# Kernel tuning notes

Hardware: AMD Instinct MI355X
Metric: run time of the kernel (lower is better)

## Reference

```python
import jax, jax.numpy as jnp
import numpy as np

B, C, F = 16384, 1000, 256
ALPHA = 10


def setup_inputs() -> dict:
    key = jax.random.key(0)
    k1, k2, k3, k4, k5 = jax.random.split(key, 5)
    logits = jax.random.normal(k1, (B, C), dtype=jnp.float32)
    features = jax.random.normal(k2, (B, F), dtype=jnp.float32)
    mean_vecs = jax.random.normal(k3, (C, F), dtype=jnp.float32)
    # Per-class Weibull (shape, loc, scale) as fit by scipy.weibull_min.fit.
    wb_shape = jax.random.uniform(k4, (C,), dtype=jnp.float32, minval=1.0, maxval=4.0)
    wb_loc = jnp.zeros((C,), dtype=jnp.float32)
    # typical tail distance for randn features/means is ~sqrt(2F) ~ 22.6
    wb_scale = jax.random.uniform(k5, (C,), dtype=jnp.float32, minval=10.0, maxval=25.0)
    return {"logits": logits, "features": features, "mean_vecs": mean_vecs,
            "wb_shape": wb_shape, "wb_loc": wb_loc, "wb_scale": wb_scale}


def reference(logits, features, mean_vecs, wb_shape, wb_loc, wb_scale):
    # Batched per-class Euclidean distances via the GEMM identity
    # ||f - m||^2 = ||f||^2 + ||m||^2 - 2 f.m  (avoids [B,C,F] intermediate).
    f2 = jnp.sum(features * features, axis=1, keepdims=True)        # [B,1]
    m2 = jnp.sum(mean_vecs * mean_vecs, axis=1)                     # [C]
    d2 = f2 + m2[None, :] - 2.0 * (features @ mean_vecs.T)          # [B,C]
    dist = jnp.sqrt(jnp.maximum(d2, 1e-12))                         # [B,C]
    # Analytic weibull_min CDF: 1 - exp(-((x - loc)/scale)^c), 0 for x <= loc.
    xp = (dist - wb_loc[None, :]) / wb_scale[None, :]
    pos = xp > 0
    xp_safe = jnp.where(pos, xp, 1.0)
    w = jnp.where(pos, 1.0 - jnp.exp(-(xp_safe ** wb_shape[None, :])), 0.0)
    # OpenMax reweighting + softmax (exp/sum-normalize as in the original).
    scores = logits * (1.0 - w ** ALPHA)                            # [B,C]
    return jax.nn.softmax(scores, axis=-1)
```

## Files before the change

kernel.cpp:

```cpp
#include <hip/hip_runtime.h>

#define NB 16384
#define NC 1000
#define NF 256

typedef _Float16 half8 __attribute__((ext_vector_type(8)));
typedef float f32x4 __attribute__((ext_vector_type(4)));

__global__ __launch_bounds__(256) void prep_kernel(
    const float* __restrict__ mean_vecs,
    const float* __restrict__ wb_shape,
    const float* __restrict__ wb_loc,
    const float* __restrict__ wb_scale,
    _Float16* __restrict__ m16f,
    float* __restrict__ pm2,
    float* __restrict__ psh,
    float* __restrict__ pli,
    float* __restrict__ pis)
{
    const int lane = threadIdx.x & 63;
    const int W = blockIdx.x * 4 + (threadIdx.x >> 6);

    if (W < 512) {
        const int gt = W >> 3, kk = W & 7;
        int cls = gt * 16 + (lane & 15);
        if (cls > NC - 1) cls = NC - 1;
        const float* src = mean_vecs + (size_t)cls * NF + kk * 32 + (lane >> 4) * 8;
        const float4 lo = *(const float4*)src;
        const float4 hi = *(const float4*)(src + 4);
        half8 h;
        h[0]=(_Float16)lo.x; h[1]=(_Float16)lo.y; h[2]=(_Float16)lo.z; h[3]=(_Float16)lo.w;
        h[4]=(_Float16)hi.x; h[5]=(_Float16)hi.y; h[6]=(_Float16)hi.z; h[7]=(_Float16)hi.w;
        *((half8*)m16f + (size_t)W * 64 + lane) = h;
    }
    if (W < NC) {
        const float4 v = *((const float4*)(mean_vecs + (size_t)W * NF) + lane);
        float s = v.x*v.x + v.y*v.y + v.z*v.z + v.w*v.w;
        #pragma unroll
        for (int off = 1; off < 64; off <<= 1) s += __shfl_xor(s, off, 64);
        if (lane == 0) {
            const float isc = 1.0f / wb_scale[W];
            pm2[W] = s;
            psh[W] = wb_shape[W];
            pli[W] = wb_loc[W] * isc;
            pis[W] = isc;
        }
    }
}

__global__ __launch_bounds__(512, 4) void score_kernel(
    const float* __restrict__ logits,
    const float* __restrict__ features,
    const _Float16* __restrict__ m16f,
    const float* __restrict__ pm2,
    const float* __restrict__ psh,
    const float* __restrict__ pli,
    const float* __restrict__ pis,
    float* __restrict__ out)
{
    __shared__ float ssum[8][16];

    const int lane = threadIdx.x & 63;
    const int wave = threadIdx.x >> 6;
    const int q    = lane >> 4;
    const int mr   = lane & 15;
    const int row  = blockIdx.x * 16 + mr;

    half8 bfrag[8];
    float f2 = 0.f;
    const float* fb = features + (size_t)row * NF;
    #pragma unroll
    for (int kk = 0; kk < 8; ++kk) {
        const float4* p = (const float4*)(fb + kk * 32 + q * 8);
        const float4 lo = p[0], hi = p[1];
        f2 += lo.x*lo.x + lo.y*lo.y + lo.z*lo.z + lo.w*lo.w
            + hi.x*hi.x + hi.y*hi.y + hi.z*hi.z + hi.w*hi.w;
        half8 b;
        b[0]=(_Float16)lo.x; b[1]=(_Float16)lo.y; b[2]=(_Float16)lo.z; b[3]=(_Float16)lo.w;
        b[4]=(_Float16)hi.x; b[5]=(_Float16)hi.y; b[6]=(_Float16)hi.z; b[7]=(_Float16)hi.w;
        bfrag[kk] = b;
    }
    f2 += __shfl_xor(f2, 16, 64);
    f2 += __shfl_xor(f2, 32, 64);

    const float LOG2E = 1.44269504088896340736f;
    float rsum = 0.f;
    f32x4 ev[8];

    const half8* mbase = (const half8*)m16f + (size_t)(wave * 8) * 8 * 64 + lane;

    #pragma unroll
    for (int t = 0; t < 8; ++t) {
        const int gt  = wave * 8 + t;
        const int cb  = gt * 16 + q * 4;
        const bool cvg = (cb <= NC - 4);
        const int cbc = cvg ? cb : (NC - 4);

        half8 a[8];
        #pragma unroll
        for (int kk = 0; kk < 8; ++kk)
            a[kk] = mbase[(size_t)(t * 8 + kk) * 64];

        f32x4 acc = {0.f, 0.f, 0.f, 0.f};
        #pragma unroll
        for (int kk = 0; kk < 8; ++kk)
            acc = __builtin_amdgcn_mfma_f32_16x16x32_f16(a[kk], bfrag[kk], acc, 0, 0, 0);

        const float4 lg  = *(const float4*)(logits + (size_t)row * NC + cbc);
        const float4 m2v = *(const float4*)(pm2 + cbc);
        const float4 shv = *(const float4*)(psh + cbc);
        const float4 liv = *(const float4*)(pli + cbc);
        const float4 iv  = *(const float4*)(pis + cbc);

        const float* m2a = (const float*)&m2v;
        const float* sha = (const float*)&shv;
        const float* lia = (const float*)&liv;
        const float* iva = (const float*)&iv;
        const float* lga = (const float*)&lg;

        #pragma unroll
        for (int j = 0; j < 4; ++j) {
            float d2   = fmaxf(f2 + m2a[j] - 2.0f * acc[j], 1e-12f);
            float dist = sqrtf(d2);
            float xp   = dist * iva[j] - lia[j];
            float xs   = fmaxf(xp, 1e-30f);
            float tt   = exp2f(sha[j] * log2f(xs));
            float w    = 1.0f - exp2f(-LOG2E * tt);
            w = (xp > 0.f) ? w : 0.f;
            float w2 = w * w, w4 = w2 * w2, w8 = w4 * w4;
            float s  = lga[j] * (1.0f - w8 * w2);
            float e  = exp2f(LOG2E * s);
            e = cvg ? e : 0.f;
            rsum += e;
            ev[t][j] = e;
        }
    }

    rsum += __shfl_xor(rsum, 16, 64);
    rsum += __shfl_xor(rsum, 32, 64);
    if (lane < 16) ssum[wave][lane] = rsum;
    __syncthreads();
    float tot = 0.f;
    #pragma unroll
    for (int w = 0; w < 8; ++w) tot += ssum[w][mr];
    const float inv = 1.0f / tot;

    #pragma unroll
    for (int t = 0; t < 8; ++t) {
        const int gt = wave * 8 + t;
        const int cb = gt * 16 + q * 4;
        if (cb <= NC - 4) {
            float4 o;
            o.x = ev[t][0] * inv; o.y = ev[t][1] * inv;
            o.z = ev[t][2] * inv; o.w = ev[t][3] * inv;
            *(float4*)(out + (size_t)row * NC + cb) = o;
        }
    }
}

extern "C" void kernel_launch(void* const* d_in, const int* in_sizes, int n_in,
                              void* d_out, int out_size, void* d_ws, size_t ws_size,
                              hipStream_t stream) {
    const float* logits    = (const float*)d_in[0];
    const float* features  = (const float*)d_in[1];
    const float* mean_vecs = (const float*)d_in[2];
    const float* wb_shape  = (const float*)d_in[3];
    const float* wb_loc    = (const float*)d_in[4];
    const float* wb_scale  = (const float*)d_in[5];
    float* out = (float*)d_out;

    _Float16* m16f = (_Float16*)d_ws;
    float* pm2 = (float*)((char*)d_ws + 524288);
    float* psh = (float*)((char*)d_ws + 524288 + 4096);
    float* pli = (float*)((char*)d_ws + 524288 + 8192);
    float* pis = (float*)((char*)d_ws + 524288 + 12288);

    prep_kernel<<<252, 256, 0, stream>>>(mean_vecs, wb_shape, wb_loc, wb_scale,
                                         m16f, pm2, psh, pli, pis);
    score_kernel<<<NB / 16, 512, 0, stream>>>(logits, features, m16f,
                                              pm2, psh, pli, pis, out);
}
```

Measured before the change: 185.5 us.

## Stage softmax numerators in LDS for coalesced row stores; prefetch next tile

The unnormalized exponentials now go into a 16x1004 shared-memory tile instead of registers. After the row sums are reduced, each wave writes two full output rows with contiguous float4 stores, replacing the scattered 16-byte-per-lane pattern. The loop also software-prefetches the next tile's mean-vector fragments and logits while the current MFMA and epilogue run. In exchange it uses about 64KB of LDS per block, which may lower occupancy below the launch bound of 4 blocks, and adds a second barrier.

```diff
diff --git a/kernel.cpp b/kernel.cpp
--- a/kernel.cpp
+++ b/kernel.cpp
@@ -3,6 +3,7 @@
 #define NB 16384
 #define NC 1000
 #define NF 256
+#define SE_STRIDE 1004
 
 typedef _Float16 half8 __attribute__((ext_vector_type(8)));
 typedef float f32x4 __attribute__((ext_vector_type(4)));
@@ -58,7 +59,9 @@
     const float* __restrict__ pis,
     float* __restrict__ out)
 {
+    __shared__ float se[16][SE_STRIDE];
     __shared__ float ssum[8][16];
+    __shared__ float sinv[16];
 
     const int lane = threadIdx.x & 63;
     const int wave = threadIdx.x >> 6;
@@ -85,28 +88,38 @@
 
     const float LOG2E = 1.44269504088896340736f;
     float rsum = 0.f;
-    f32x4 ev[8];
 
     const half8* mbase = (const half8*)m16f + (size_t)(wave * 8) * 8 * 64 + lane;
+    const float* lrow  = logits + (size_t)row * NC;
+
+    half8 a[8];
+    #pragma unroll
+    for (int kk = 0; kk < 8; ++kk)
+        a[kk] = mbase[kk * 64];
+    float4 lg = *(const float4*)(lrow + (wave * 128 + q * 4));
 
     #pragma unroll
     for (int t = 0; t < 8; ++t) {
-        const int gt  = wave * 8 + t;
-        const int cb  = gt * 16 + q * 4;
+        const int gt   = wave * 8 + t;
+        const int cb   = gt * 16 + q * 4;
         const bool cvg = (cb <= NC - 4);
-        const int cbc = cvg ? cb : (NC - 4);
-
-        half8 a[8];
-        #pragma unroll
-        for (int kk = 0; kk < 8; ++kk)
-            a[kk] = mbase[(size_t)(t * 8 + kk) * 64];
+        const int cbc  = cvg ? cb : (NC - 4);
 
         f32x4 acc = {0.f, 0.f, 0.f, 0.f};
         #pragma unroll
         for (int kk = 0; kk < 8; ++kk)
             acc = __builtin_amdgcn_mfma_f32_16x16x32_f16(a[kk], bfrag[kk], acc, 0, 0, 0);
 
-        const float4 lg  = *(const float4*)(logits + (size_t)row * NC + cbc);
+        float4 lgn = lg;
+        if (t < 7) {
+            #pragma unroll
+            for (int kk = 0; kk < 8; ++kk)
+                a[kk] = mbase[(size_t)((t + 1) * 8 + kk) * 64];
+            const int cbn  = cb + 16;
+            const int cbnc = (cbn <= NC - 4) ? cbn : (NC - 4);
+            lgn = *(const float4*)(lrow + cbnc);
+        }
+
         const float4 m2v = *(const float4*)(pm2 + cbc);
         const float4 shv = *(const float4*)(psh + cbc);
         const float4 liv = *(const float4*)(pli + cbc);
@@ -118,6 +131,7 @@
         const float* iva = (const float*)&iv;
         const float* lga = (const float*)&lg;
 
+        f32x4 o;
         #pragma unroll
         for (int j = 0; j < 4; ++j) {
             float d2   = fmaxf(f2 + m2a[j] - 2.0f * acc[j], 1e-12f);
@@ -132,28 +146,40 @@
             float e  = exp2f(LOG2E * s);
             e = cvg ? e : 0.f;
             rsum += e;
-            ev[t][j] = e;
-        }
+            o[j] = e;
+        }
+
+        if (cvg)
+            *(f32x4*)&se[mr][cb] = o;
+
+        lg = lgn;
     }
 
     rsum += __shfl_xor(rsum, 16, 64);
     rsum += __shfl_xor(rsum, 32, 64);
     if (lane < 16) ssum[wave][lane] = rsum;
     __syncthreads();
-    float tot = 0.f;
-    #pragma unroll
-    for (int w = 0; w < 8; ++w) tot += ssum[w][mr];
-    const float inv = 1.0f / tot;
-
-    #pragma unroll
-    for (int t = 0; t < 8; ++t) {
-        const int gt = wave * 8 + t;
-        const int cb = gt * 16 + q * 4;
-        if (cb <= NC - 4) {
-            float4 o;
-            o.x = ev[t][0] * inv; o.y = ev[t][1] * inv;
-            o.z = ev[t][2] * inv; o.w = ev[t][3] * inv;
-            *(float4*)(out + (size_t)row * NC + cb) = o;
+    if (wave == 0 && lane < 16) {
+        float tot = 0.f;
+        #pragma unroll
+        for (int w = 0; w < 8; ++w) tot += ssum[w][lane];
+        sinv[lane] = 1.0f / tot;
+    }
+    __syncthreads();
+
+    #pragma unroll
+    for (int rr = 0; rr < 2; ++rr) {
+        const int r = wave * 2 + rr;
+        const float inv = sinv[r];
+        float* orow = out + (size_t)(blockIdx.x * 16 + r) * NC;
+        #pragma unroll
+        for (int i = 0; i < 4; ++i) {
+            const int idx = i * 64 + lane;
+            if (idx < 250) {
+                float4 v = *(const float4*)&se[r][idx * 4];
+                v.x *= inv; v.y *= inv; v.z *= inv; v.w *= inv;
+                *(float4*)(orow + idx * 4) = v;
+            }
         }
     }
 }
```

After: 183.7 us. About the same (-1.0%).
